# Kernel optimization log

Hardware: AMD Instinct MI355X
Metric: run time of the kernel (lower is better)

The kernel has to match this reference:

```python
import jax, jax.numpy as jnp
import numpy as np
import math

LOG_GAMMA_3_2 = math.log(math.gamma(1.5))


def setup_inputs() -> dict:
    key = jax.random.key(0)
    k1, k2, k3 = jax.random.split(key, 3)
    M = 262144
    N = 128
    n_phases = 4
    n_int = n_phases * (n_phases - 1) // 2  # 6 interfaces, none ignored
    # data: u is the mean-intensity channel, v > 0 is the gradient-magnitude channel
    u = jax.random.normal(k1, (M,), jnp.float32) * 0.3 + 0.5
    v = jax.random.uniform(k2, (M,), jnp.float32, minval=1e-3, maxval=0.5)
    # one fresh uniform draw of N MC samples per interface (as in the torch loop)
    uniform_eps = jax.random.uniform(k3, (n_int, N), jnp.float32)
    # learned parameters, matching reset_params()
    I = jnp.linspace(0.0, 1.0, n_phases).astype(jnp.float32)
    W = jnp.zeros((n_int + n_phases,), jnp.float32)
    sigma_b = jnp.asarray(2.0, jnp.float32)
    sigma_n = jnp.asarray(0.1, jnp.float32)
    d = jnp.asarray(2.0, jnp.float32)
    r = jnp.asarray(0.0, jnp.float32)
    return dict(u=u, v=v, uniform_eps=uniform_eps, I=I, W=W,
                sigma_b=sigma_b, sigma_n=sigma_n, d=d, r=r)


def _log_ive_half(z):
    # ive(0.5, z) = sqrt(2/(pi z)) * sinh(z) * exp(-z) = sqrt(2/(pi z)) * (1 - exp(-2z)) / 2
    return 0.5 * jnp.log(2.0 / (math.pi * z)) - math.log(2.0) + jnp.log1p(-jnp.exp(-2.0 * z))


def reference(u, v, uniform_eps, I, W, sigma_b, sigma_n, d, r):
    M = u.shape[0]
    rho = jnp.tanh(r)
    sig_eff = sigma_n * jnp.sqrt(1.0 - rho)      # sigma_n * sqrt(1-rho)
    sn2 = sigma_n ** 2 * (1.0 - rho)
    log_w = jax.nn.log_softmax(W)

    # ---- interior components: [n_phases, M] ----
    lp_interior = (math.log(2.0) + 2.0 * jnp.log(v)[None, :] - LOG_GAMMA_3_2
                   - 3.0 * jnp.log(sig_eff) - (v[None, :] / sig_eff) ** 2
                   - jnp.log(sigma_n) - 0.5 * math.log(2.0 * math.pi)
                   - 0.5 * ((u[None, :] - I[:, None]) / sigma_n) ** 2)

    # ---- interface components via MC logsumexp ----
    # torch loop order (Ia < Ib, I ascending) == row-major triu order
    ia, ib = np.triu_indices(I.shape[0], k=1)
    Ia_all, Ib_all = I[ia], I[ib]  # [n_int]

    def interface_lp(Ia, Ib, eps):
        # eps: [N] uniforms -> importance samples In from p(I)
        ux = eps * 2.0 * d * sigma_b - d * sigma_b
        In = (jax.lax.erf(ux / (math.sqrt(2.0) * sigma_b)) + 1.0) * 0.5 * (Ib - Ia) + Ia
        In_ = In[:, None]  # [N, 1]
        # log p(u | I)
        lp_u = (-jnp.log(sigma_n) - 0.5 * math.log(2.0 * math.pi)
                - 0.5 * ((u[None, :] - In_) / sigma_n) ** 2)
        # G(I)
        G_ = ((Ib - Ia) / jnp.sqrt(2.0 * math.pi * sigma_b ** 2)
              * jnp.exp(-jax.scipy.special.erfinv(2.0 * (In_ - Ia) / (Ib - Ia) - 1.0) ** 2))
        z = 2.0 * v[None, :] * G_ / sn2  # [N, M]
        # log p(v | I), with exp-scaled modified Bessel of order 0.5 in closed form
        lp_v = (math.log(2.0) - 2.0 * jnp.log(sig_eff) + 1.5 * jnp.log(v)[None, :]
                - 0.5 * jnp.log(G_) + _log_ive_half(z) + z
                - (v[None, :] ** 2 + G_ ** 2) / sn2)
        N = eps.shape[0]
        return jax.scipy.special.logsumexp(lp_u + lp_v, axis=0) - math.log(N)  # [M]

    lp_interface = jax.vmap(interface_lp)(Ia_all, Ib_all, uniform_eps)  # [n_int, M]

    log_p = jnp.concatenate([lp_interior, lp_interface], axis=0)  # [n_phases+n_int, M]
    log_p_u_v = jax.scipy.special.logsumexp(log_w[:, None] + log_p, axis=0)  # [M]
    return -jnp.sum(log_p_u_v) / M
```

## Files before the change

kernel.cpp:

```cpp
#include <hip/hip_runtime.h>
#include <math.h>

#define L2E_F 1.4426950408889634f
#define LN2_F 0.69314718055994531f

#define NU 256
#define NT 64
#define GU0 (-2.2f)
#define GHU (5.4f / 255.0f)
#define GT0 (-10.3f)
#define GHT (9.75f / 63.0f)
#define WS_CONST 16
#define WS_NEED ((size_t)(WS_CONST + NU * NT) * sizeof(float))

typedef float v2f __attribute__((ext_vector_type(2)));

static __device__ __forceinline__ float fexp2(float x) { return __builtin_amdgcn_exp2f(x); }
static __device__ __forceinline__ float flog2(float x) { return __builtin_amdgcn_logf(x); }
static __device__ __forceinline__ v2f vfma(v2f a, v2f b, v2f c) {
  return __builtin_elementwise_fma(a, b, c);
}


__launch_bounds__(256)
__global__ void build_kernel(const float* __restrict__ eps, const float* __restrict__ Iarr,
                             const float* __restrict__ Warr,
                             const float* __restrict__ psb, const float* __restrict__ psn,
                             const float* __restrict__ pdd, const float* __restrict__ prr,
                             float* __restrict__ ws, float* __restrict__ out) {
  __shared__ float sIn[768], sQ[768], sD[768];
  __shared__ float sPart[4][64];
  const int tid = threadIdx.x;

  const float sb = psb[0], sn = psn[0], dd = pdd[0], rv = prr[0];
  const float rho = tanhf(rv);
  const float sig_eff = sn * sqrtf(1.0f - rho);
  const float sn2 = sn * sn * (1.0f - rho);
  const float inv_sn2 = 1.0f / sn2;
  const float inv_2snsq = 0.5f / (sn * sn);

  float wmax = -1e30f;
  for (int k = 0; k < 10; ++k) wmax = fmaxf(wmax, Warr[k]);
  float wsum = 0.0f;
  for (int k = 0; k < 10; ++k) wsum += expf(Warr[k] - wmax);
  const float lse_w = wmax + logf(wsum);
  const float ln128 = logf(128.0f);
  const float I0 = Iarr[0], I1 = Iarr[1], I2 = Iarr[2], I3 = Iarr[3];

  for (int t = tid; t < 768; t += 256) {
    const int j = t >> 7;
    const float Ia = (j < 3) ? I0 : ((j < 5) ? I1 : I2);
    const float Ib = (j == 0) ? I1 : ((j == 1 || j == 3) ? I2 : I3);
    const float e = eps[t];
    const float ux = fmaf(e, 2.0f * dd * sb, -dd * sb);
    const float arg = ux * (0.70710678f / sb);
    const float In = fmaf((erff(arg) + 1.0f) * 0.5f, (Ib - Ia), Ia);
    const float G = (Ib - Ia) * (0.39894228f / sb) * expf(-arg * arg);
    const float lw = Warr[4 + j] - lse_w;
    const float q = -logf(G) - G * G * inv_sn2 + lw - ln128;
    sIn[t] = In;
    sQ[t] = q * L2E_F;
    sD[t] = (2.0f * G * inv_sn2) * L2E_F;
  }
  __syncthreads();

  const float cB2 = inv_2snsq * L2E_F;
  const int q4 = tid >> 6;
  const int lane = tid & 63;
  const int cell = blockIdx.x * 64 + lane;
  const int iu = cell & (NU - 1);
  const int it = cell >> 8;
  const float uc = GU0 + GHU * (float)iu;
  const float vc = fexp2(fmaf(GHT, (float)it, GT0));
  float s1 = 0.0f, s2 = 0.0f;
  const int tbase = q4 * 192;
#pragma unroll 4
  for (int i = 0; i < 192; ++i) {
    const int t = tbase + i;
    const float du = uc - sIn[t];
    const float P = fmaf(du * du, -cB2, sQ[t]);
    const float z = vc * sD[t];
    s1 += fexp2(P + z);
    s2 += fexp2(P - z);
  }
  sPart[q4][lane] = s1 - s2;
  __syncthreads();
  if (q4 == 0) {
    const float F = (sPart[0][lane] + sPart[1][lane]) + (sPart[2][lane] + sPart[3][lane]);
    ws[WS_CONST + cell] = flog2(fmaxf(F, 1e-35f));
  }
  if (blockIdx.x == 0 && tid == 0) {
    ws[0] = cB2;
    ws[1] = inv_sn2 * L2E_F;
    const float Cs_ln = -logf(sn) - 0.91893853f - logf(sig_eff) - 0.57236494f;
    ws[2] = Cs_ln * L2E_F;
    const float LG_ln = -0.12078224f;
#pragma unroll
    for (int p = 0; p < 4; ++p) {
      const float Ip = (p == 0) ? I0 : ((p == 1) ? I1 : ((p == 2) ? I2 : I3));
      const float lw = Warr[p] - lse_w;
      const float bI_ln = lw + 0.69314718f - LG_ln - 3.0f * logf(sig_eff)
                          - logf(sn) - 0.91893853f - Cs_ln - Ip * Ip * inv_2snsq;
      ws[3 + p] = (bI_ln + Ip * Ip * inv_2snsq) * L2E_F;
      ws[7 + p] = Ip;
    }
    out[0] = 0.0f;
  }
}

__launch_bounds__(256)
__global__ void eval_kernel(const float* __restrict__ U, const float* __restrict__ V,
                            const float* __restrict__ ws, float* __restrict__ out,
                            float scale) {
  const int tid = threadIdx.x;
  const int m = blockIdx.x * 256 + tid;
  const float cB = ws[0], cA = ws[1], Cs2 = ws[2];
  float qI[4], Ip[4];
#pragma unroll
  for (int k = 0; k < 4; ++k) { qI[k] = ws[3 + k]; Ip[k] = ws[7 + k]; }

  const float u = U[m], v = V[m];
  const float l2v = flog2(v);

  float xu = (u - GU0) * (1.0f / GHU);
  xu = fminf(fmaxf(xu, 1.0f), (float)(NU - 2) - 1e-3f);
  float xt = (l2v - GT0) * (1.0f / GHT);
  xt = fminf(fmaxf(xt, 1.0f), (float)(NT - 2) - 1e-3f);
  const float fiu = floorf(xu), fit_ = floorf(xt);
  const int iu = (int)fiu, it = (int)fit_;
  const float fu = xu - fiu, ft = xt - fit_;

  float wu0, wu1, wu2, wu3, wt0, wt1, wt2, wt3;
  {
    const float f = fu, f2 = f * f, f3 = f2 * f;
    wu0 = -0.5f * f3 + f2 - 0.5f * f;
    wu1 = 1.5f * f3 - 2.5f * f2 + 1.0f;
    wu2 = -1.5f * f3 + 2.0f * f2 + 0.5f * f;
    wu3 = 0.5f * f3 - 0.5f * f2;
  }
  {
    const float f = ft, f2 = f * f, f3 = f2 * f;
    wt0 = -0.5f * f3 + f2 - 0.5f * f;
    wt1 = 1.5f * f3 - 2.5f * f2 + 1.0f;
    wt2 = -1.5f * f3 + 2.0f * f2 + 0.5f * f;
    wt3 = 0.5f * f3 - 0.5f * f2;
  }

  const float* T = ws + WS_CONST + (it - 1) * NU + (iu - 1);
  float r0 = wu0 * T[0] + wu1 * T[1] + wu2 * T[2] + wu3 * T[3];
  T += NU;
  float r1 = wu0 * T[0] + wu1 * T[1] + wu2 * T[2] + wu3 * T[3];
  T += NU;
  float r2 = wu0 * T[0] + wu1 * T[1] + wu2 * T[2] + wu3 * T[3];
  T += NU;
  float r3 = wu0 * T[0] + wu1 * T[1] + wu2 * T[2] + wu3 * T[3];
  const float Fi = ((wt0 * r0 + wt1 * r1) + (wt2 * r2 + wt3 * r3));

  float accI = 0.0f;
#pragma unroll
  for (int k = 0; k < 4; ++k) {
    const float du = u - Ip[k];
    accI += fexp2(fmaf(du * du, -cB, qI[k]) + l2v);
  }
  float tot = fexp2(Fi) + accI;
  tot = fmaxf(tot, 1e-30f);
  float lp = Cs2 + fmaf(-v * v, cA, l2v) + flog2(tot);

#pragma unroll
  for (int o = 1; o < 64; o <<= 1) lp += __shfl_xor(lp, o, 64);
  __shared__ float wsum4[4];
  if ((tid & 63) == 0) wsum4[tid >> 6] = lp;
  __syncthreads();
  if (tid == 0) atomicAdd(out, ((wsum4[0] + wsum4[1]) + (wsum4[2] + wsum4[3])) * scale);
}


__global__ void setup_kernel(const float* __restrict__ eps, const float* __restrict__ Iarr,
                             const float* __restrict__ Warr,
                             const float* __restrict__ psb, const float* __restrict__ psn,
                             const float* __restrict__ pdd, const float* __restrict__ prr,
                             float* __restrict__ ws, float* __restrict__ out) {
  const int tid = threadIdx.x;
  const float sb = psb[0], sn = psn[0], dd = pdd[0], rv = prr[0];
  const float rho = tanhf(rv);
  const float sig_eff = sn * sqrtf(1.0f - rho);
  const float sn2 = sn * sn * (1.0f - rho);
  const float inv_sn2 = 1.0f / sn2;
  const float inv_2snsq = 0.5f / (sn * sn);
  float wmax = -1e30f;
  for (int k = 0; k < 10; ++k) wmax = fmaxf(wmax, Warr[k]);
  float wsum = 0.0f;
  for (int k = 0; k < 10; ++k) wsum += expf(Warr[k] - wmax);
  const float lse_w = wmax + logf(wsum);
  const float LG_ln = -0.12078224f;
  const float Cs_ln = -logf(sn) - 0.91893853f - logf(sig_eff) - 0.57236494f;
  const float ln128 = logf(128.0f);
  const float I0 = Iarr[0], I1 = Iarr[1], I2 = Iarr[2], I3 = Iarr[3];
  for (int t = tid; t < 768; t += 256) {
    const int j = t >> 7;
    const float Ia = (j < 3) ? I0 : ((j < 5) ? I1 : I2);
    const float Ib = (j == 0) ? I1 : ((j == 1 || j == 3) ? I2 : I3);
    const float e = eps[t];
    const float ux = fmaf(e, 2.0f * dd * sb, -dd * sb);
    const float arg = ux * (0.70710678f / sb);
    const float In = fmaf((erff(arg) + 1.0f) * 0.5f, (Ib - Ia), Ia);
    const float G = (Ib - Ia) * (0.39894228f / sb) * expf(-arg * arg);
    const float lw = Warr[4 + j] - lse_w;
    const float q = -logf(G) - G * G * inv_sn2 + lw - ln128;
    ws[16 + (t >> 1) * 4 + (t & 1)] = In;
    ws[16 + (t >> 1) * 4 + 2 + (t & 1)] = q * L2E_F;
    ws[1552 + t] = (2.0f * G * inv_sn2) * L2E_F;
  }
  if (tid == 0) {
    ws[0] = inv_2snsq * L2E_F;
    ws[1] = inv_sn2 * L2E_F;
    ws[2] = Cs_ln * L2E_F;
#pragma unroll
    for (int p = 0; p < 4; ++p) {
      const float Ip = (p == 0) ? I0 : ((p == 1) ? I1 : ((p == 2) ? I2 : I3));
      const float lw = Warr[p] - lse_w;
      const float bI_ln = lw + 0.69314718f - LG_ln - 3.0f * logf(sig_eff)
                          - logf(sn) - 0.91893853f - Cs_ln - Ip * Ip * inv_2snsq;
      ws[3 + p] = (bI_ln + Ip * Ip * inv_2snsq) * L2E_F;
      ws[7 + p] = Ip;
    }
    out[0] = 0.0f;
  }
}

__launch_bounds__(256, 8)
__global__ void main_kernel(const float* __restrict__ U, const float* __restrict__ V,
                            const float* __restrict__ ws, float* __restrict__ out,
                            float scale) {
  __shared__ float4 sT[576];
  __shared__ float sums[4][128];
  const int tid = threadIdx.x;
  const int q = tid >> 6;
  const int lane = tid & 63;
  const float4* gT = (const float4*)(ws + 16);
  for (int k = tid; k < 576; k += 256) sT[k] = gT[k];
  const float cB = ws[0], cA = ws[1], Cs2 = ws[2];
  float qI[4], Ip[4];
#pragma unroll
  for (int k = 0; k < 4; ++k) { qI[k] = ws[3 + k]; Ip[k] = ws[7 + k]; }
  __syncthreads();
  const int m0 = blockIdx.x * 128 + lane;
  const float u0 = U[m0], v0 = V[m0];
  const float u1 = U[m0 + 64], v1 = V[m0 + 64];
  const v2f u0_2 = {u0, u0}, vv0 = {v0, v0}, mv0 = {-v0, -v0};
  const v2f u1_2 = {u1, u1}, vv1 = {v1, v1}, mv1 = {-v1, -v1};
  const v2f mcB2 = {-cB, -cB};
  const float4* Qh = sT + q * 96;
  const float4* Dh = sT + 384 + q * 48;
  v2f aP0 = {0.f, 0.f}, aM0 = {0.f, 0.f}, aP1 = {0.f, 0.f}, aM1 = {0.f, 0.f};
#pragma unroll 2
  for (int i = 0; i < 48; ++i) {
    const float4 A0 = Qh[2 * i];
    const float4 A1 = Qh[2 * i + 1];
    const float4 Dp = Dh[i];
    v2f In0, q0, In1, q1, d0, d1;
    In0.x = A0.x; In0.y = A0.y; q0.x = A0.z; q0.y = A0.w;
    In1.x = A1.x; In1.y = A1.y; q1.x = A1.z; q1.y = A1.w;
    d0.x = Dp.x; d0.y = Dp.y; d1.x = Dp.z; d1.y = Dp.w;
    {
      const v2f du0 = u0_2 - In0, du1 = u0_2 - In1;
      const v2f P0 = vfma(du0 * du0, mcB2, q0), P1 = vfma(du1 * du1, mcB2, q1);
      const v2f E1 = vfma(vv0, d0, P0), E2 = vfma(mv0, d0, P0);
      const v2f E3 = vfma(vv0, d1, P1), E4 = vfma(mv0, d1, P1);
      v2f X1, X2, X3, X4;
      X1.x = fexp2(E1.x); X1.y = fexp2(E1.y);
      X2.x = fexp2(E2.x); X2.y = fexp2(E2.y);
      X3.x = fexp2(E3.x); X3.y = fexp2(E3.y);
      X4.x = fexp2(E4.x); X4.y = fexp2(E4.y);
      aP0 += X1; aM0 += X2; aP0 += X3; aM0 += X4;
    }
    {
      const v2f du0 = u1_2 - In0, du1 = u1_2 - In1;
      const v2f P0 = vfma(du0 * du0, mcB2, q0), P1 = vfma(du1 * du1, mcB2, q1);
      const v2f E1 = vfma(vv1, d0, P0), E2 = vfma(mv1, d0, P0);
      const v2f E3 = vfma(vv1, d1, P1), E4 = vfma(mv1, d1, P1);
      v2f X1, X2, X3, X4;
      X1.x = fexp2(E1.x); X1.y = fexp2(E1.y);
      X2.x = fexp2(E2.x); X2.y = fexp2(E2.y);
      X3.x = fexp2(E3.x); X3.y = fexp2(E3.y);
      X4.x = fexp2(E4.x); X4.y = fexp2(E4.y);
      aP1 += X1; aM1 += X2; aP1 += X3; aM1 += X4;
    }
  }
  sums[q][lane]      = (aP0.x + aP0.y) - (aM0.x + aM0.y);
  sums[q][lane + 64] = (aP1.x + aP1.y) - (aM1.x + aM1.y);
  __syncthreads();
  if (q == 0) {
    float lp = 0.0f;
#pragma unroll
    for (int pp = 0; pp < 2; ++pp) {
      const int idx = lane + 64 * pp;
      const float u = (pp == 0) ? u0 : u1;
      const float v = (pp == 0) ? v0 : v1;
      const float l2v = flog2(v);
      float accI = 0.0f;
#pragma unroll
      for (int k = 0; k < 4; ++k) {
        const float du = u - Ip[k];
        accI += fexp2(__builtin_fmaf(du * du, -cB, qI[k]) + l2v);
      }
      float tot = (sums[0][idx] + sums[1][idx]) + (sums[2][idx] + sums[3][idx]) + accI;
      tot = fmaxf(tot, 1e-30f);
      lp += Cs2 + __builtin_fmaf(-v * v, cA, l2v) + flog2(tot);
    }
#pragma unroll
    for (int o = 1; o < 64; o <<= 1) lp += __shfl_xor(lp, o, 64);
    if (lane == 0) atomicAdd(out, lp * scale);
  }
}

extern "C" void kernel_launch(void* const* d_in, const int* in_sizes, int n_in,
                              void* d_out, int out_size, void* d_ws, size_t ws_size,
                              hipStream_t stream) {
  const float* u   = (const float*)d_in[0];
  const float* v   = (const float*)d_in[1];
  const float* eps = (const float*)d_in[2];
  const float* I   = (const float*)d_in[3];
  const float* W   = (const float*)d_in[4];
  const float* sb  = (const float*)d_in[5];
  const float* sn  = (const float*)d_in[6];
  const float* dd  = (const float*)d_in[7];
  const float* rr  = (const float*)d_in[8];
  const int M = in_sizes[0];
  float* ws = (float*)d_ws;
  const float scale = -LN2_F / (float)M;

  if (ws_size >= WS_NEED) {
    build_kernel<<<(NU * NT) / 64, 256, 0, stream>>>(eps, I, W, sb, sn, dd, rr,
                                                     ws, (float*)d_out);
    eval_kernel<<<M / 256, 256, 0, stream>>>(u, v, ws, (float*)d_out, scale);
  } else {
    setup_kernel<<<1, 256, 0, stream>>>(eps, I, W, sb, sn, dd, rr, ws, (float*)d_out);
    main_kernel<<<M / 128, 256, 0, stream>>>(u, v, ws, (float*)d_out, scale);
  }
}
```

Measured before the change: 98.66 us.

## Fold interior components into lookup table and split build across more blocks

The four interior Gaussian terms are now folded into the precomputed 2D log-table (evaluated at grid nodes and scaled by v), so the eval kernel only interpolates the table and skips the per-element exp2 terms and the final log2. The build kernel now computes 16 cells per block with 16 threads each over 48 samples, launching four times as many blocks to raise parallelism during table construction. The trade-off is accuracy: the interior terms, which are sharp Gaussians in u, are now cubically interpolated in log space rather than computed exactly.

```diff
diff --git a/kernel.cpp b/kernel.cpp
--- a/kernel.cpp
+++ b/kernel.cpp
@@ -29,7 +29,7 @@
                              const float* __restrict__ pdd, const float* __restrict__ prr,
                              float* __restrict__ ws, float* __restrict__ out) {
   __shared__ float sIn[768], sQ[768], sD[768];
-  __shared__ float sPart[4][64];
+  __shared__ float sPart[16][17];
   const int tid = threadIdx.x;
 
   const float sb = psb[0], sn = psn[0], dd = pdd[0], rv = prr[0];
@@ -45,7 +45,10 @@
   for (int k = 0; k < 10; ++k) wsum += expf(Warr[k] - wmax);
   const float lse_w = wmax + logf(wsum);
   const float ln128 = logf(128.0f);
+  const float LG_ln = -0.12078224f;
+  const float Cs_ln = -logf(sn) - 0.91893853f - logf(sig_eff) - 0.57236494f;
   const float I0 = Iarr[0], I1 = Iarr[1], I2 = Iarr[2], I3 = Iarr[3];
+  const float cB2 = inv_2snsq * L2E_F;
 
   for (int t = tid; t < 768; t += 256) {
     const int j = t >> 7;
@@ -64,46 +67,54 @@
   }
   __syncthreads();
 
-  const float cB2 = inv_2snsq * L2E_F;
-  const int q4 = tid >> 6;
-  const int lane = tid & 63;
-  const int cell = blockIdx.x * 64 + lane;
+  const int c = tid >> 4;
+  const int sub = tid & 15;
+  const int cell = blockIdx.x * 16 + c;
   const int iu = cell & (NU - 1);
   const int it = cell >> 8;
   const float uc = GU0 + GHU * (float)iu;
   const float vc = fexp2(fmaf(GHT, (float)it, GT0));
   float s1 = 0.0f, s2 = 0.0f;
-  const int tbase = q4 * 192;
-#pragma unroll 4
-  for (int i = 0; i < 192; ++i) {
-    const int t = tbase + i;
+  const int tb = sub * 48;
+#pragma unroll 6
+  for (int i = 0; i < 48; ++i) {
+    const int t = tb + i;
     const float du = uc - sIn[t];
     const float P = fmaf(du * du, -cB2, sQ[t]);
     const float z = vc * sD[t];
     s1 += fexp2(P + z);
     s2 += fexp2(P - z);
   }
-  sPart[q4][lane] = s1 - s2;
-  __syncthreads();
-  if (q4 == 0) {
-    const float F = (sPart[0][lane] + sPart[1][lane]) + (sPart[2][lane] + sPart[3][lane]);
-    ws[WS_CONST + cell] = flog2(fmaxf(F, 1e-35f));
-  }
-  if (blockIdx.x == 0 && tid == 0) {
-    ws[0] = cB2;
-    ws[1] = inv_sn2 * L2E_F;
-    const float Cs_ln = -logf(sn) - 0.91893853f - logf(sig_eff) - 0.57236494f;
-    ws[2] = Cs_ln * L2E_F;
-    const float LG_ln = -0.12078224f;
+  sPart[c][sub] = s1 - s2;
+  __syncthreads();
+
+  if (tid < 16) {
+    const int cc = tid;
+    float F = 0.0f;
+#pragma unroll
+    for (int k = 0; k < 16; ++k) F += sPart[cc][k];
+    const int cell2 = blockIdx.x * 16 + cc;
+    const int iu2 = cell2 & (NU - 1);
+    const int it2 = cell2 >> 8;
+    const float uc2 = GU0 + GHU * (float)iu2;
+    const float vc2 = fexp2(fmaf(GHT, (float)it2, GT0));
+    float J = 0.0f;
 #pragma unroll
     for (int p = 0; p < 4; ++p) {
       const float Ip = (p == 0) ? I0 : ((p == 1) ? I1 : ((p == 2) ? I2 : I3));
       const float lw = Warr[p] - lse_w;
       const float bI_ln = lw + 0.69314718f - LG_ln - 3.0f * logf(sig_eff)
                           - logf(sn) - 0.91893853f - Cs_ln - Ip * Ip * inv_2snsq;
-      ws[3 + p] = (bI_ln + Ip * Ip * inv_2snsq) * L2E_F;
-      ws[7 + p] = Ip;
-    }
+      const float qI = (bI_ln + Ip * Ip * inv_2snsq) * L2E_F;
+      const float du = uc2 - Ip;
+      J += fexp2(fmaf(du * du, -cB2, qI));
+    }
+    const float tot = F + vc2 * J;
+    ws[WS_CONST + cell2] = flog2(fmaxf(tot, 1e-35f));
+  }
+  if (blockIdx.x == 0 && tid == 0) {
+    ws[0] = inv_sn2 * L2E_F;
+    ws[1] = Cs_ln * L2E_F;
     out[0] = 0.0f;
   }
 }
@@ -114,10 +125,7 @@
                             float scale) {
   const int tid = threadIdx.x;
   const int m = blockIdx.x * 256 + tid;
-  const float cB = ws[0], cA = ws[1], Cs2 = ws[2];
-  float qI[4], Ip[4];
-#pragma unroll
-  for (int k = 0; k < 4; ++k) { qI[k] = ws[3 + k]; Ip[k] = ws[7 + k]; }
+  const float cA = ws[0], Cs2 = ws[1];
 
   const float u = U[m], v = V[m];
   const float l2v = flog2(v);
@@ -154,17 +162,9 @@
   float r2 = wu0 * T[0] + wu1 * T[1] + wu2 * T[2] + wu3 * T[3];
   T += NU;
   float r3 = wu0 * T[0] + wu1 * T[1] + wu2 * T[2] + wu3 * T[3];
-  const float Fi = ((wt0 * r0 + wt1 * r1) + (wt2 * r2 + wt3 * r3));
-
-  float accI = 0.0f;
-#pragma unroll
-  for (int k = 0; k < 4; ++k) {
-    const float du = u - Ip[k];
-    accI += fexp2(fmaf(du * du, -cB, qI[k]) + l2v);
-  }
-  float tot = fexp2(Fi) + accI;
-  tot = fmaxf(tot, 1e-30f);
-  float lp = Cs2 + fmaf(-v * v, cA, l2v) + flog2(tot);
+  const float Fi = (wt0 * r0 + wt1 * r1) + (wt2 * r2 + wt3 * r3);
+
+  float lp = Cs2 + fmaf(-v * v, cA, l2v) + Fi;
 
 #pragma unroll
   for (int o = 1; o < 64; o <<= 1) lp += __shfl_xor(lp, o, 64);
@@ -331,7 +331,7 @@
   const float scale = -LN2_F / (float)M;
 
   if (ws_size >= WS_NEED) {
-    build_kernel<<<(NU * NT) / 64, 256, 0, stream>>>(eps, I, W, sb, sn, dd, rr,
+    build_kernel<<<(NU * NT) / 16, 256, 0, stream>>>(eps, I, W, sb, sn, dd, rr,
                                                      ws, (float*)d_out);
     eval_kernel<<<M / 256, 256, 0, stream>>>(u, v, ws, (float*)d_out, scale);
   } else {
```

Measured after the change: 103.1 us. 4.5% more time.
